# Kernel optimization log

Hardware: AMD Instinct MI355X
Metric: run time of the kernel (lower is better)

## Reference

```python
import jax, jax.numpy as jnp
import numpy as np

B, H, D = 16, 32, 128          # batch, heads, head_dim
NB, BS, MB = 1024, 16, 128     # num cache blocks, block_size, max blocks per seq
HIDDEN = H * D
EPS = 1e-6


def setup_inputs() -> dict:
    key = jax.random.key(0)
    ks = jax.random.split(key, 5)
    return {
        "hidden_states": jax.random.normal(ks[0], (B, HIDDEN), dtype=jnp.float32),
        "key_cache": jax.random.normal(ks[1], (NB, BS, H, D), dtype=jnp.float32),
        "value_cache": jax.random.normal(ks[2], (NB, BS, H, D), dtype=jnp.float32),
        "block_tables": jax.random.randint(ks[3], (B, MB), 0, NB, dtype=jnp.int32),
        "context_lens": jax.random.randint(ks[4], (B,), 1, MB * BS + 1, dtype=jnp.int32),
        "rms_weight": jnp.ones((HIDDEN,), dtype=jnp.float32),
    }


def reference(hidden_states, key_cache, value_cache, block_tables, context_lens, rms_weight):
    bsz = hidden_states.shape[0]
    nb, bs, h, d = key_cache.shape
    scale = 1.0 / np.sqrt(d).astype(np.float32)

    residual = hidden_states
    # RMSNorm
    x = hidden_states
    norm = x * jax.lax.rsqrt(jnp.mean(x * x, axis=-1, keepdims=True) + EPS) * rms_weight
    q = norm.reshape(bsz, h, d)  # [B, H, D] single decode token per sequence

    # Paged KV gather: block_tables [B, MB] indexes into cache blocks
    keys = key_cache[block_tables].reshape(bsz, -1, h, d)    # [B, S, H, D], S = MB*BS
    vals = value_cache[block_tables].reshape(bsz, -1, h, d)  # [B, S, H, D]
    s = keys.shape[1]

    scores = jnp.einsum('bhd,bshd->bhs', q, keys) * scale    # [B, H, S]
    valid = jnp.arange(s, dtype=jnp.int32)[None, :] < context_lens[:, None]  # [B, S]
    scores = jnp.where(valid[:, None, :], scores, -jnp.inf)
    probs = jax.nn.softmax(scores, axis=-1)
    attn = jnp.einsum('bhs,bshd->bhd', probs, vals).reshape(bsz, h * d)

    return residual + attn
```

## Files before the change

kernel.cpp:

```cpp
#include <hip/hip_runtime.h>
#include <math.h>

#define BATCH 16
#define NHEAD 32
#define HDIM 128
#define HIDDEN 4096
#define BS 16
#define MB 128
#define EPS 1e-6f
#define NWORK 8
#define SPLIT 8

#define Q_FLOATS (BATCH * HIDDEN)
#define M_OFF Q_FLOATS
#define L_OFF (M_OFF + BATCH * NHEAD * SPLIT)
#define A_OFF (L_OFF + BATCH * NHEAD * SPLIT)

__global__ __launch_bounds__(256) void rmsnorm_kernel(const float* __restrict__ x,
                                                      const float* __restrict__ w,
                                                      float* __restrict__ q) {
    int b = blockIdx.x;
    int tid = threadIdx.x;
    const float4* xr = (const float4*)(x + (size_t)b * HIDDEN);
    float4 xs[4];
    float ss = 0.f;
#pragma unroll
    for (int i = 0; i < 4; i++) {
        float4 v = xr[tid + i * 256];
        xs[i] = v;
        ss += v.x * v.x + v.y * v.y + v.z * v.z + v.w * v.w;
    }
#pragma unroll
    for (int m = 32; m >= 1; m >>= 1) ss += __shfl_xor(ss, m, 64);
    __shared__ float red[4];
    int wave = tid >> 6;
    if ((tid & 63) == 0) red[wave] = ss;
    __syncthreads();
    float tot = red[0] + red[1] + red[2] + red[3];
    float rstd = rsqrtf(tot * (1.0f / HIDDEN) + EPS);

    const float4* wr = (const float4*)w;
    float4* qr = (float4*)(q + (size_t)b * HIDDEN);
#pragma unroll
    for (int i = 0; i < 4; i++) {
        float4 v = xs[i];
        float4 ww = wr[tid + i * 256];
        float4 o;
        o.x = v.x * rstd * ww.x;
        o.y = v.y * rstd * ww.y;
        o.z = v.z * rstd * ww.z;
        o.w = v.w * rstd * ww.w;
        qr[tid + i * 256] = o;
    }
}

__global__ __launch_bounds__(256) void attn_partial_kernel(const float* __restrict__ ws,
                                                           const float* __restrict__ kc,
                                                           const float* __restrict__ vc,
                                                           const int* __restrict__ bt,
                                                           const int* __restrict__ cl,
                                                           float* __restrict__ pm,
                                                           float* __restrict__ pl,
                                                           float* __restrict__ pacc) {
    const int h = blockIdx.x;
    const int b = blockIdx.y;
    const int si = blockIdx.z;
    const int tid = threadIdx.x;
    const int w = tid >> 5;
    const int lane = tid & 31;

    __shared__ int s_bt[MB];
    __shared__ float s_m[NWORK];
    __shared__ float s_l[NWORK];
    __shared__ float s_acc[NWORK][HDIM];

    const int L = cl[b];
    const int chunk = (L + SPLIT - 1) / SPLIT;
    const int s0 = si * chunk;
    const int s1 = min(s0 + chunk, L);

    if (tid < MB) s_bt[tid] = bt[b * MB + tid];
    float4 q4 = *(const float4*)(ws + (size_t)b * HIDDEN + h * HDIM + 4 * lane);
    __syncthreads();

    const float scale = 0.08838834764831845f;
    float m = -INFINITY;
    float l = 0.f;
    float4 acc = make_float4(0.f, 0.f, 0.f, 0.f);

    int s = s0 + w;
    for (; s + NWORK < s1; s += 2 * NWORK) {
        int sB = s + NWORK;
        size_t offA = ((((size_t)s_bt[s >> 4] * BS + (s & 15)) * NHEAD + h) * HDIM) + 4 * lane;
        size_t offB = ((((size_t)s_bt[sB >> 4] * BS + (sB & 15)) * NHEAD + h) * HDIM) + 4 * lane;
        float4 kA = *(const float4*)(kc + offA);
        float4 kB = *(const float4*)(kc + offB);
        float4 vA = *(const float4*)(vc + offA);
        float4 vB = *(const float4*)(vc + offB);
        float dA = kA.x * q4.x + kA.y * q4.y + kA.z * q4.z + kA.w * q4.w;
        float dB = kB.x * q4.x + kB.y * q4.y + kB.z * q4.z + kB.w * q4.w;
#pragma unroll
        for (int msk = 16; msk >= 1; msk >>= 1) {
            dA += __shfl_xor(dA, msk, 64);
            dB += __shfl_xor(dB, msk, 64);
        }
        float scA = dA * scale, scB = dB * scale;
        float mn = fmaxf(m, fmaxf(scA, scB));
        float alpha = __expf(m - mn);
        float p0 = __expf(scA - mn);
        float p1 = __expf(scB - mn);
        l = l * alpha + p0 + p1;
        acc.x = acc.x * alpha + p0 * vA.x + p1 * vB.x;
        acc.y = acc.y * alpha + p0 * vA.y + p1 * vB.y;
        acc.z = acc.z * alpha + p0 * vA.z + p1 * vB.z;
        acc.w = acc.w * alpha + p0 * vA.w + p1 * vB.w;
        m = mn;
    }
    for (; s < s1; s += NWORK) {
        size_t off = ((((size_t)s_bt[s >> 4] * BS + (s & 15)) * NHEAD + h) * HDIM) + 4 * lane;
        float4 k4 = *(const float4*)(kc + off);
        float4 v4 = *(const float4*)(vc + off);
        float dot = k4.x * q4.x + k4.y * q4.y + k4.z * q4.z + k4.w * q4.w;
#pragma unroll
        for (int msk = 16; msk >= 1; msk >>= 1) dot += __shfl_xor(dot, msk, 64);
        float score = dot * scale;
        float mn = fmaxf(m, score);
        float alpha = __expf(m - mn);
        float p = __expf(score - mn);
        l = l * alpha + p;
        acc.x = acc.x * alpha + p * v4.x;
        acc.y = acc.y * alpha + p * v4.y;
        acc.z = acc.z * alpha + p * v4.z;
        acc.w = acc.w * alpha + p * v4.w;
        m = mn;
    }

    *((float4*)&s_acc[w][4 * lane]) = acc;
    if (lane == 0) {
        s_m[w] = m;
        s_l[w] = l;
    }
    __syncthreads();

    if (tid < HDIM) {
        float M = -INFINITY;
#pragma unroll
        for (int i = 0; i < NWORK; i++) M = fmaxf(M, s_m[i]);
        size_t pbase = ((size_t)(b * NHEAD + h) * SPLIT + si);
        if (M == -INFINITY) {
            if (tid == 0) { pm[pbase] = -INFINITY; pl[pbase] = 0.f; }
            pacc[pbase * HDIM + tid] = 0.f;
        } else {
            float Ls = 0.f, A = 0.f;
#pragma unroll
            for (int i = 0; i < NWORK; i++) {
                float sc = __expf(s_m[i] - M);
                Ls += s_l[i] * sc;
                A += s_acc[i][tid] * sc;
            }
            if (tid == 0) { pm[pbase] = M; pl[pbase] = Ls; }
            pacc[pbase * HDIM + tid] = A;
        }
    }
}

__global__ __launch_bounds__(128) void attn_combine_kernel(const float* __restrict__ pm,
                                                           const float* __restrict__ pl,
                                                           const float* __restrict__ pacc,
                                                           const float* __restrict__ resid,
                                                           float* __restrict__ out) {
    const int h = blockIdx.x;
    const int b = blockIdx.y;
    const int tid = threadIdx.x;
    size_t pbase = (size_t)(b * NHEAD + h) * SPLIT;

    float M = -INFINITY;
#pragma unroll
    for (int i = 0; i < SPLIT; i++) M = fmaxf(M, pm[pbase + i]);
    float Ls = 0.f, A = 0.f;
#pragma unroll
    for (int i = 0; i < SPLIT; i++) {
        float sc = __expf(pm[pbase + i] - M);
        Ls += pl[pbase + i] * sc;
        A += pacc[(pbase + i) * HDIM + tid] * sc;
    }
    size_t oi = (size_t)b * HIDDEN + h * HDIM + tid;
    out[oi] = resid[oi] + A / Ls;
}

extern "C" void kernel_launch(void* const* d_in, const int* in_sizes, int n_in,
                              void* d_out, int out_size, void* d_ws, size_t ws_size,
                              hipStream_t stream) {
    const float* hs = (const float*)d_in[0];
    const float* kc = (const float*)d_in[1];
    const float* vc = (const float*)d_in[2];
    const int* bt = (const int*)d_in[3];
    const int* cl = (const int*)d_in[4];
    const float* rw = (const float*)d_in[5];
    float* out = (float*)d_out;
    float* ws = (float*)d_ws;
    float* q = ws;
    float* pm = ws + M_OFF;
    float* pl = ws + L_OFF;
    float* pacc = ws + A_OFF;

    rmsnorm_kernel<<<BATCH, 256, 0, stream>>>(hs, rw, q);
    attn_partial_kernel<<<dim3(NHEAD, BATCH, SPLIT), 256, 0, stream>>>(q, kc, vc, bt, cl,
                                                                       pm, pl, pacc);
    attn_combine_kernel<<<dim3(NHEAD, BATCH), 128, 0, stream>>>(pm, pl, pacc, hs, out);
}
```

Measured before the change: 494.6 us.

## Process one cache page per block across all heads, fuse RMSNorm into attention

```diff
diff --git a/kernel.cpp b/kernel.cpp
--- a/kernel.cpp
+++ b/kernel.cpp
@@ -8,183 +8,127 @@
 #define BS 16
 #define MB 128
 #define EPS 1e-6f
-#define NWORK 8
-#define SPLIT 8
+#define SPLIT 128
 
-#define Q_FLOATS (BATCH * HIDDEN)
-#define M_OFF Q_FLOATS
-#define L_OFF (M_OFF + BATCH * NHEAD * SPLIT)
-#define A_OFF (L_OFF + BATCH * NHEAD * SPLIT)
+#define PCOUNT (BATCH * NHEAD * SPLIT)
+#define PL_OFF PCOUNT
+#define PA_OFF (2 * PCOUNT)
 
-__global__ __launch_bounds__(256) void rmsnorm_kernel(const float* __restrict__ x,
-                                                      const float* __restrict__ w,
-                                                      float* __restrict__ q) {
-    int b = blockIdx.x;
-    int tid = threadIdx.x;
+__global__ __launch_bounds__(256) void attn_page_kernel(
+    const float* __restrict__ x, const float* __restrict__ rw,
+    const float* __restrict__ kc, const float* __restrict__ vc,
+    const int* __restrict__ bt, const int* __restrict__ cl,
+    float* __restrict__ pm, float* __restrict__ pl, float* __restrict__ pacc) {
+    const int si = blockIdx.x;
+    const int b = blockIdx.y;
+    const int L = cl[b];
+    const int nsp = (L + BS - 1) >> 4;
+    if (si >= nsp) return;
+    const int nt = min(BS, L - (si << 4));
+    const int tid = threadIdx.x;
+    const int hw = tid >> 5;
+    const int lane = tid & 31;
+
     const float4* xr = (const float4*)(x + (size_t)b * HIDDEN);
-    float4 xs[4];
+    const float4* wr = (const float4*)rw;
+    float4 qf[4];
     float ss = 0.f;
 #pragma unroll
     for (int i = 0; i < 4; i++) {
-        float4 v = xr[tid + i * 256];
-        xs[i] = v;
+        float4 v = xr[tid + 256 * i];
+        qf[i] = v;
         ss += v.x * v.x + v.y * v.y + v.z * v.z + v.w * v.w;
     }
 #pragma unroll
     for (int m = 32; m >= 1; m >>= 1) ss += __shfl_xor(ss, m, 64);
     __shared__ float red[4];
-    int wave = tid >> 6;
-    if ((tid & 63) == 0) red[wave] = ss;
+    if ((tid & 63) == 0) red[tid >> 6] = ss;
     __syncthreads();
-    float tot = red[0] + red[1] + red[2] + red[3];
-    float rstd = rsqrtf(tot * (1.0f / HIDDEN) + EPS);
-
-    const float4* wr = (const float4*)w;
-    float4* qr = (float4*)(q + (size_t)b * HIDDEN);
+    const float rstd = rsqrtf((red[0] + red[1] + red[2] + red[3]) * (1.0f / HIDDEN) + EPS);
 #pragma unroll
     for (int i = 0; i < 4; i++) {
-        float4 v = xs[i];
-        float4 ww = wr[tid + i * 256];
-        float4 o;
-        o.x = v.x * rstd * ww.x;
-        o.y = v.y * rstd * ww.y;
-        o.z = v.z * rstd * ww.z;
-        o.w = v.w * rstd * ww.w;
-        qr[tid + i * 256] = o;
+        float4 wv = wr[tid + 256 * i];
+        qf[i].x *= rstd * wv.x;
+        qf[i].y *= rstd * wv.y;
+        qf[i].z *= rstd * wv.z;
+        qf[i].w *= rstd * wv.w;
+    }
+
+    const int pg = bt[b * MB + si];
+    const float4* kb = (const float4*)(kc + (size_t)pg * (BS * HIDDEN));
+    const float4* vb = (const float4*)(vc + (size_t)pg * (BS * HIDDEN));
+
+    const float scale = 0.08838834764831845f;
+    float m0[4], l0[4];
+    float4 acc[4];
+#pragma unroll
+    for (int i = 0; i < 4; i++) {
+        m0[i] = -INFINITY;
+        l0[i] = 0.f;
+        acc[i] = make_float4(0.f, 0.f, 0.f, 0.f);
+    }
+
+    for (int t = 0; t < nt; ++t) {
+        const float4* krow = kb + (size_t)t * (HIDDEN / 4);
+        const float4* vrow = vb + (size_t)t * (HIDDEN / 4);
+        float4 k4[4], v4[4];
+#pragma unroll
+        for (int i = 0; i < 4; i++) {
+            k4[i] = krow[tid + 256 * i];
+            v4[i] = vrow[tid + 256 * i];
+        }
+#pragma unroll
+        for (int i = 0; i < 4; i++) {
+            float d = k4[i].x * qf[i].x + k4[i].y * qf[i].y + k4[i].z * qf[i].z +
+                      k4[i].w * qf[i].w;
+#pragma unroll
+            for (int msk = 16; msk >= 1; msk >>= 1) d += __shfl_xor(d, msk, 64);
+            float sc = d * scale;
+            float mn = fmaxf(m0[i], sc);
+            float al = __expf(m0[i] - mn);
+            float p = __expf(sc - mn);
+            l0[i] = l0[i] * al + p;
+            acc[i].x = acc[i].x * al + p * v4[i].x;
+            acc[i].y = acc[i].y * al + p * v4[i].y;
+            acc[i].z = acc[i].z * al + p * v4[i].z;
+            acc[i].w = acc[i].w * al + p * v4[i].w;
+            m0[i] = mn;
+        }
+    }
+
+#pragma unroll
+    for (int i = 0; i < 4; i++) {
+        const int h = hw + 8 * i;
+        const size_t pb = (size_t)(b * NHEAD + h) * SPLIT + si;
+        if (lane == 0) {
+            pm[pb] = m0[i];
+            pl[pb] = l0[i];
+        }
+        *(float4*)(pacc + pb * HDIM + 4 * lane) = acc[i];
     }
 }
 
-__global__ __launch_bounds__(256) void attn_partial_kernel(const float* __restrict__ ws,
-                                                           const float* __restrict__ kc,
-                                                           const float* __restrict__ vc,
-                                                           const int* __restrict__ bt,
-                                                           const int* __restrict__ cl,
-                                                           float* __restrict__ pm,
-                                                           float* __restrict__ pl,
-                                                           float* __restrict__ pacc) {
-    const int h = blockIdx.x;
-    const int b = blockIdx.y;
-    const int si = blockIdx.z;
-    const int tid = threadIdx.x;
-    const int w = tid >> 5;
-    const int lane = tid & 31;
-
-    __shared__ int s_bt[MB];
-    __shared__ float s_m[NWORK];
-    __shared__ float s_l[NWORK];
-    __shared__ float s_acc[NWORK][HDIM];
-
-    const int L = cl[b];
-    const int chunk = (L + SPLIT - 1) / SPLIT;
-    const int s0 = si * chunk;
-    const int s1 = min(s0 + chunk, L);
-
-    if (tid < MB) s_bt[tid] = bt[b * MB + tid];
-    float4 q4 = *(const float4*)(ws + (size_t)b * HIDDEN + h * HDIM + 4 * lane);
-    __syncthreads();
-
-    const float scale = 0.08838834764831845f;
-    float m = -INFINITY;
-    float l = 0.f;
-    float4 acc = make_float4(0.f, 0.f, 0.f, 0.f);
-
-    int s = s0 + w;
-    for (; s + NWORK < s1; s += 2 * NWORK) {
-        int sB = s + NWORK;
-        size_t offA = ((((size_t)s_bt[s >> 4] * BS + (s & 15)) * NHEAD + h) * HDIM) + 4 * lane;
-        size_t offB = ((((size_t)s_bt[sB >> 4] * BS + (sB & 15)) * NHEAD + h) * HDIM) + 4 * lane;
-        float4 kA = *(const float4*)(kc + offA);
-        float4 kB = *(const float4*)(kc + offB);
-        float4 vA = *(const float4*)(vc + offA);
-        float4 vB = *(const float4*)(vc + offB);
-        float dA = kA.x * q4.x + kA.y * q4.y + kA.z * q4.z + kA.w * q4.w;
-        float dB = kB.x * q4.x + kB.y * q4.y + kB.z * q4.z + kB.w * q4.w;
-#pragma unroll
-        for (int msk = 16; msk >= 1; msk >>= 1) {
-            dA += __shfl_xor(dA, msk, 64);
-            dB += __shfl_xor(dB, msk, 64);
-        }
-        float scA = dA * scale, scB = dB * scale;
-        float mn = fmaxf(m, fmaxf(scA, scB));
-        float alpha = __expf(m - mn);
-        float p0 = __expf(scA - mn);
-        float p1 = __expf(scB - mn);
-        l = l * alpha + p0 + p1;
-        acc.x = acc.x * alpha + p0 * vA.x + p1 * vB.x;
-        acc.y = acc.y * alpha + p0 * vA.y + p1 * vB.y;
-        acc.z = acc.z * alpha + p0 * vA.z + p1 * vB.z;
-        acc.w = acc.w * alpha + p0 * vA.w + p1 * vB.w;
-        m = mn;
-    }
-    for (; s < s1; s += NWORK) {
-        size_t off = ((((size_t)s_bt[s >> 4] * BS + (s & 15)) * NHEAD + h) * HDIM) + 4 * lane;
-        float4 k4 = *(const float4*)(kc + off);
-        float4 v4 = *(const float4*)(vc + off);
-        float dot = k4.x * q4.x + k4.y * q4.y + k4.z * q4.z + k4.w * q4.w;
-#pragma unroll
-        for (int msk = 16; msk >= 1; msk >>= 1) dot += __shfl_xor(dot, msk, 64);
-        float score = dot * scale;
-        float mn = fmaxf(m, score);
-        float alpha = __expf(m - mn);
-        float p = __expf(score - mn);
-        l = l * alpha + p;
-        acc.x = acc.x * alpha + p * v4.x;
-        acc.y = acc.y * alpha + p * v4.y;
-        acc.z = acc.z * alpha + p * v4.z;
-        acc.w = acc.w * alpha + p * v4.w;
-        m = mn;
-    }
-
-    *((float4*)&s_acc[w][4 * lane]) = acc;
-    if (lane == 0) {
-        s_m[w] = m;
-        s_l[w] = l;
-    }
-    __syncthreads();
-
-    if (tid < HDIM) {
-        float M = -INFINITY;
-#pragma unroll
-        for (int i = 0; i < NWORK; i++) M = fmaxf(M, s_m[i]);
-        size_t pbase = ((size_t)(b * NHEAD + h) * SPLIT + si);
-        if (M == -INFINITY) {
-            if (tid == 0) { pm[pbase] = -INFINITY; pl[pbase] = 0.f; }
-            pacc[pbase * HDIM + tid] = 0.f;
-        } else {
-            float Ls = 0.f, A = 0.f;
-#pragma unroll
-            for (int i = 0; i < NWORK; i++) {
-                float sc = __expf(s_m[i] - M);
-                Ls += s_l[i] * sc;
-                A += s_acc[i][tid] * sc;
-            }
-            if (tid == 0) { pm[pbase] = M; pl[pbase] = Ls; }
-            pacc[pbase * HDIM + tid] = A;
-        }
-    }
-}
-
-__global__ __launch_bounds__(128) void attn_combine_kernel(const float* __restrict__ pm,
-                                                           const float* __restrict__ pl,
-                                                           const float* __restrict__ pacc,
-                                                           const float* __restrict__ resid,
-                                                           float* __restrict__ out) {
+__global__ __launch_bounds__(128) void attn_combine_kernel(
+    const float* __restrict__ pm, const float* __restrict__ pl,
+    const float* __restrict__ pacc, const float* __restrict__ resid,
+    const int* __restrict__ cl, float* __restrict__ out) {
     const int h = blockIdx.x;
     const int b = blockIdx.y;
     const int tid = threadIdx.x;
-    size_t pbase = (size_t)(b * NHEAD + h) * SPLIT;
+    const int L = cl[b];
+    const int nsp = (L + BS - 1) >> 4;
+    const size_t pb0 = (size_t)(b * NHEAD + h) * SPLIT;
 
     float M = -INFINITY;
-#pragma unroll
-    for (int i = 0; i < SPLIT; i++) M = fmaxf(M, pm[pbase + i]);
+    for (int si = 0; si < nsp; ++si) M = fmaxf(M, pm[pb0 + si]);
     float Ls = 0.f, A = 0.f;
-#pragma unroll
-    for (int i = 0; i < SPLIT; i++) {
-        float sc = __expf(pm[pbase + i] - M);
-        Ls += pl[pbase + i] * sc;
-        A += pacc[(pbase + i) * HDIM + tid] * sc;
+#pragma unroll 4
+    for (int si = 0; si < nsp; ++si) {
+        float sc = __expf(pm[pb0 + si] - M);
+        Ls += pl[pb0 + si] * sc;
+        A += pacc[(pb0 + si) * HDIM + tid] * sc;
     }
-    size_t oi = (size_t)b * HIDDEN + h * HDIM + tid;
+    const size_t oi = (size_t)b * HIDDEN + h * HDIM + tid;
     out[oi] = resid[oi] + A / Ls;
 }
 
@@ -199,13 +143,11 @@
     const float* rw = (const float*)d_in[5];
     float* out = (float*)d_out;
     float* ws = (float*)d_ws;
-    float* q = ws;
-    float* pm = ws + M_OFF;
-    float* pl = ws + L_OFF;
-    float* pacc = ws + A_OFF;
+    float* pm = ws;
+    float* pl = ws + PL_OFF;
+    float* pacc = ws + PA_OFF;
 
-    rmsnorm_kernel<<<BATCH, 256, 0, stream>>>(hs, rw, q);
-    attn_partial_kernel<<<dim3(NHEAD, BATCH, SPLIT), 256, 0, stream>>>(q, kc, vc, bt, cl,
-                                                                       pm, pl, pacc);
-    attn_combine_kernel<<<dim3(NHEAD, BATCH), 128, 0, stream>>>(pm, pl, pacc, hs, out);
+    attn_page_kernel<<<dim3(SPLIT, BATCH), 256, 0, stream>>>(hs, rw, kc, vc, bt, cl,
+                                                             pm, pl, pacc);
+    attn_combine_kernel<<<dim3(NHEAD, BATCH), 128, 0, stream>>>(pm, pl, pacc, hs, cl, out);
 }
```

Measured after the change: 513.0 us. 3.7% more time.
